# Kernel optimization log

Hardware: AMD Instinct MI355X
Metric: run time of the kernel (lower is better)

Reference implementation:

```python
import jax, jax.numpy as jnp
import numpy as np

N_BINS = 32
R = 1.2
BOUND = 50.0
_m = N_BINS // 2
_x1L = BOUND * (R - 1.0) / (R ** _m - 1.0)
X1L = _x1L / (2.0 * BOUND)  # x1L rescaled to the [0,1] domain
_idx = np.arange(N_BINS + 1, dtype=np.float64) - _m
_xr = np.where(_idx >= 0, (1.0 - R ** _idx) / (1.0 - R), (1.0 - R ** np.abs(_idx)) / (1.0 - R))
_xr = np.where(_idx >= 0, _x1L * _xr, -_x1L * _xr)
_xr = (_xr + BOUND) / (2.0 * BOUND)
MESH = np.concatenate([[0.0], _xr[1:-1], [1.0]]).astype(np.float32)   # (n_bins+1,)
ESIZE = (MESH[1:] - MESH[:-1]).astype(np.float32)                     # (n_bins,)

N, D = 524288, 64

def setup_inputs() -> dict:
    key = jax.random.key(0)
    k1, k2, k3, k4 = jax.random.split(key, 4)
    return {
        "x": jax.random.normal(k1, (N, D), jnp.float32) * 5.0,
        "logdet": jnp.zeros((N, 1), jnp.float32),
        "p": jax.random.normal(k2, (N_BINS - 1, D), jnp.float32) * 0.1,
        "b": jax.random.normal(k3, (1, D), jnp.float32) * 0.1,
        "logs": jax.random.normal(k4, (1, D), jnp.float32) * 0.1,
    }

def reference(x, logdet, p, b, logs):
    mesh = jnp.asarray(MESH)              # (n_bins+1,)
    es = jnp.asarray(ESIZE)               # (n_bins,)
    # ---- actnorm (data_init already done; b_init = logs_init = 0) ----
    ls = jnp.clip(logs, -5.0, 5.0)
    z = (x + b) * jnp.exp(ls)             # (N, D)
    logdet = logdet + jnp.sum(ls)
    # ---- pdf normalization ----
    ep = jnp.exp(p)                                         # (n_bins-1, D)
    w = ((es[:-1] + es[1:]) / 2.0)[:, None]                 # trapezoid weights
    px = ep * ((1.0 - es[0]) / jnp.sum(ep * w, 0, keepdims=True))
    ones = jnp.ones((1, p.shape[1]), p.dtype)
    pdf = jnp.concatenate([ones, px, ones], 0)              # (n_bins+1, D)
    cell = (pdf[:-1] + pdf[1:]) / 2.0 * es[:, None]         # (n_bins, D)
    F_ref = jnp.concatenate([jnp.zeros_like(ones), jnp.cumsum(cell, 0)[:-1]], 0)  # (n_bins, D)
    # ---- forward CDF: analytic bin index + batched gather + quadratic interp ----
    xs = (z + BOUND) / (2.0 * BOUND)                        # map to [0,1]
    sgn = jnp.sign(xs - 0.5)
    mfl = jnp.floor(jnp.log(jnp.abs(xs - 0.5) * (R - 1.0) / X1L + 1.0) / np.log(R))
    k = jnp.where(sgn >= 0, N_BINS // 2 + mfl, N_BINS // 2 - mfl - 1).astype(jnp.int32)
    cover = (k * (k - (N_BINS - 1))) <= 0                   # inside the mesh?
    k = jnp.clip(k, 0, N_BINS - 1)
    v1 = jnp.take_along_axis(pdf, k, 0)                     # pdf at left node
    v2 = jnp.take_along_axis(pdf, k + 1, 0)                 # pdf at right node
    xmodi = xs - mesh[k]
    h = es[k]
    F_pre = jnp.take_along_axis(F_ref, k, 0)
    y = jnp.where(cover, F_pre + xmodi * xmodi * 0.5 * (v2 - v1) / h + xmodi * v1, xs)
    dlog = jnp.where(cover, xmodi * (v2 - v1) / h + v1, 1.0)
    logdet = logdet + jnp.sum(jnp.log(dlog), axis=1, keepdims=True)
    out = y * 2.0 * BOUND - BOUND
    return out, logdet
```

## Files before the change

### kernel.cpp

```cpp
#include <hip/hip_runtime.h>
#include <math.h>

#define NBINS 32
#define DCOLS 64

#define WS_A     0
#define WS_B     2048
#define WS_C     4096
#define WS_S     6144
#define WS_T     6208
#define WS_SUMLS 6272

__global__ __launch_bounds__(64) void precompute_kernel(
    const float* __restrict__ p, const float* __restrict__ b,
    const float* __restrict__ logs, float* __restrict__ ws)
{
  const int d = threadIdx.x;

  double powr[17];
  {
    double rp = 1.0;
    for (int i = 0; i <= 16; i++) { powr[i] = rp; rp *= 1.2; }
  }
  const double x1L = 50.0 * 0.2 / (powr[16] - 1.0);
  float meshf[NBINS + 1];
  for (int i = 0; i <= NBINS; i++) {
    int idx = i - 16;
    int a = idx >= 0 ? idx : -idx;
    double xr = (1.0 - powr[a]) / (1.0 - 1.2);
    xr = (idx >= 0) ? x1L * xr : -x1L * xr;
    meshf[i] = (float)((xr + 50.0) / 100.0);
  }
  meshf[0] = 0.0f;
  meshf[NBINS] = 1.0f;
  float esf[NBINS];
  for (int i = 0; i < NBINS; i++) esf[i] = meshf[i + 1] - meshf[i];

  float ls = logs[d];
  ls = fminf(fmaxf(ls, -5.0f), 5.0f);
  const float s = expf(ls);
  const float bd = b[d];

  float ep[NBINS - 1];
  float denom = 0.0f;
  for (int j = 0; j < NBINS - 1; j++) {
    ep[j] = expf(p[j * DCOLS + d]);
    denom += ep[j] * ((esf[j] + esf[j + 1]) * 0.5f);
  }
  const float fnorm = (1.0f - esf[0]) / denom;
  float pdf[NBINS + 1];
  pdf[0] = 1.0f;
  pdf[NBINS] = 1.0f;
  for (int j = 0; j < NBINS - 1; j++) pdf[j + 1] = ep[j] * fnorm;

  float F = 0.0f;
  for (int k = 0; k < NBINS; k++) {
    const double v1 = (double)pdf[k];
    const double v2 = (double)pdf[k + 1];
    const double h  = (double)esf[k];
    const double m  = (double)meshf[k];
    const double c2 = 0.5 * (v2 - v1) / h;
    const double c1 = v1;
    const double A  = (double)F - c1 * m + c2 * m * m;
    const double B  = c1 - 2.0 * c2 * m;
    ws[WS_A + k * DCOLS + d] = (float)A;
    ws[WS_B + k * DCOLS + d] = (float)B;
    ws[WS_C + k * DCOLS + d] = (float)c2;
    const float cell = 0.5f * (pdf[k] + pdf[k + 1]) * esf[k];
    F += cell;
  }

  ws[WS_S + d] = (float)((double)s * 0.01);
  ws[WS_T + d] = (float)((double)bd * (double)s * 0.01 + 0.5);

  float sum = ls;
  for (int m = 1; m < 64; m <<= 1) sum += __shfl_xor(sum, m, 64);
  if (d == 0) ws[WS_SUMLS] = sum;
}

__device__ __forceinline__ void proc4(
    const float4 xv, const float4 S4, const float4 T4,
    const float* __restrict__ sA, const float* __restrict__ sB,
    const float* __restrict__ sC, int c0, float C1, float INVL2R,
    float4& res, float& prod)
{
  float xs_[4] = { fmaf(xv.x, S4.x, T4.x), fmaf(xv.y, S4.y, T4.y),
                   fmaf(xv.z, S4.z, T4.z), fmaf(xv.w, S4.w, T4.w) };
  float r_[4];
  float pr = 1.0f;
#pragma unroll
  for (int i = 0; i < 4; i++) {
    const float xs = xs_[i];
    const float a  = fabsf(xs - 0.5f);
    const float u  = __log2f(fmaf(a, C1, 1.0f)) * INVL2R;
    const float mfl = floorf(u);
    const float kf  = (xs >= 0.5f) ? (16.0f + mfl) : (15.0f - mfl);
    const int k = (int)kf;
    const bool cover = (k >= 0) && (k <= NBINS - 1);
    const int kc = k < 0 ? 0 : (k > NBINS - 1 ? NBINS - 1 : k);
    const int idx = kc * DCOLS + c0 + i;
    const float Av = sA[idx];
    const float Bv = sB[idx];
    const float Cv = sC[idx];
    const float y  = cover ? fmaf(xs, fmaf(xs, Cv, Bv), Av) : xs;
    const float dl = cover ? fmaf(xs, 2.0f * Cv, Bv) : 1.0f;
    r_[i] = fmaf(y, 100.0f, -50.0f);
    pr *= dl;
  }
  res = make_float4(r_[0], r_[1], r_[2], r_[3]);
  prod = pr;
}

__global__ __launch_bounds__(256) void fwd_kernel(
    const float* __restrict__ x, const float* __restrict__ logdet_in,
    const float* __restrict__ ws, float* __restrict__ out,
    float* __restrict__ logdet_out, int nrows, float C1, float INVL2R)
{
  __shared__ float sA[NBINS * DCOLS];
  __shared__ float sB[NBINS * DCOLS];
  __shared__ float sC[NBINS * DCOLS];
  {
    const float4* wsv = (const float4*)(ws);
    float4* sAv = (float4*)sA;
    float4* sBv = (float4*)sB;
    float4* sCv = (float4*)sC;
    for (int i = threadIdx.x; i < (NBINS * DCOLS) / 4; i += 256) {
      sAv[i] = wsv[(WS_A / 4) + i];
      sBv[i] = wsv[(WS_B / 4) + i];
      sCv[i] = wsv[(WS_C / 4) + i];
    }
  }
  const int lane = threadIdx.x & 63;
  const int wid  = threadIdx.x >> 6;
  const int cg   = lane & 15;
  const int rs   = lane >> 4;
  const int c0   = cg * 4;
  const float4 S4 = *(const float4*)(ws + WS_S + c0);
  const float4 T4 = *(const float4*)(ws + WS_T + c0);
  const float sumls = ws[WS_SUMLS];
  __syncthreads();

  const int gw = blockIdx.x * 4 + wid;
  const int nw = gridDim.x * 4;

  for (int r0 = gw * 8; r0 < nrows; r0 += nw * 8) {
    const int rA = r0 + rs;
    const int rB = r0 + 4 + rs;
    const float4 xA = *(const float4*)(x + (size_t)rA * DCOLS + c0);
    const float4 xB = *(const float4*)(x + (size_t)rB * DCOLS + c0);

    float4 resA, resB;
    float pA, pB;
    proc4(xA, S4, T4, sA, sB, sC, c0, C1, INVL2R, resA, pA);
    proc4(xB, S4, T4, sA, sB, sC, c0, C1, INVL2R, resB, pB);

    *(float4*)(out + (size_t)rA * DCOLS + c0) = resA;
    *(float4*)(out + (size_t)rB * DCOLS + c0) = resB;

#pragma unroll
    for (int m = 1; m < 16; m <<= 1) {
      pA *= __shfl_xor(pA, m, 64);
      pB *= __shfl_xor(pB, m, 64);
    }
    if (cg == 0) {
      logdet_out[rA] = logdet_in[rA] + sumls + logf(pA);
      logdet_out[rB] = logdet_in[rB] + sumls + logf(pB);
    }
  }
}

extern "C" void kernel_launch(void* const* d_in, const int* in_sizes, int n_in,
                              void* d_out, int out_size, void* d_ws, size_t ws_size,
                              hipStream_t stream) {
  const float* x      = (const float*)d_in[0];
  const float* logdet = (const float*)d_in[1];
  const float* p      = (const float*)d_in[2];
  const float* b      = (const float*)d_in[3];
  const float* logs   = (const float*)d_in[4];
  float* out = (float*)d_out;
  float* ws  = (float*)d_ws;

  const int N = in_sizes[0] / DCOLS;
  float* logdet_out = out + (size_t)N * DCOLS;

  precompute_kernel<<<1, 64, 0, stream>>>(p, b, logs, ws);

  double Rm = 1.0;
  for (int i = 0; i < 16; i++) Rm *= 1.2;
  const double x1L = 50.0 * (1.2 - 1.0) / (Rm - 1.0);
  const double X1L = x1L / 100.0;
  const float C1      = (float)((1.2 - 1.0) / X1L);
  const float INVL2R  = (float)(1.0 / log2(1.2));

  const int grid = 2048;
  fwd_kernel<<<grid, 256, 0, stream>>>(x, logdet, ws, out, logdet_out, N,
                                       C1, INVL2R);
}
```

Baseline: 250.9 us.

## Swizzle LDS coefficient tables and process four row groups per iteration

Coefficient tables are stored with a column swizzle (d -> (d&3)*16 + d/4). Within a float4 component, the 16 column-group lanes then read consecutive LDS words instead of a stride of 4, which is meant to cut bank conflicts on the per-element gathers. The main loop also handles 16 rows per wave per iteration instead of 8, giving four independent loads in flight per lane. The wider unroll raises register use and halves the number of loop iterations per wave.

Result: no change. 248.9 us (-0.8%).

```diff
diff --git a/kernel.cpp b/kernel.cpp
--- a/kernel.cpp
+++ b/kernel.cpp
@@ -11,11 +11,14 @@
 #define WS_T     6208
 #define WS_SUMLS 6272
 
+__device__ __forceinline__ int swz(int d) { return ((d & 3) << 4) | (d >> 2); }
+
 __global__ __launch_bounds__(64) void precompute_kernel(
     const float* __restrict__ p, const float* __restrict__ b,
     const float* __restrict__ logs, float* __restrict__ ws)
 {
   const int d = threadIdx.x;
+  const int ds = swz(d);
 
   double powr[17];
   {
@@ -63,9 +66,9 @@
     const double c1 = v1;
     const double A  = (double)F - c1 * m + c2 * m * m;
     const double B  = c1 - 2.0 * c2 * m;
-    ws[WS_A + k * DCOLS + d] = (float)A;
-    ws[WS_B + k * DCOLS + d] = (float)B;
-    ws[WS_C + k * DCOLS + d] = (float)c2;
+    ws[WS_A + k * DCOLS + ds] = (float)A;
+    ws[WS_B + k * DCOLS + ds] = (float)B;
+    ws[WS_C + k * DCOLS + ds] = (float)c2;
     const float cell = 0.5f * (pdf[k] + pdf[k + 1]) * esf[k];
     F += cell;
   }
@@ -81,7 +84,7 @@
 __device__ __forceinline__ void proc4(
     const float4 xv, const float4 S4, const float4 T4,
     const float* __restrict__ sA, const float* __restrict__ sB,
-    const float* __restrict__ sC, int c0, float C1, float INVL2R,
+    const float* __restrict__ sC, int cg, float C1, float INVL2R,
     float4& res, float& prod)
 {
   float xs_[4] = { fmaf(xv.x, S4.x, T4.x), fmaf(xv.y, S4.y, T4.y),
@@ -98,7 +101,7 @@
     const int k = (int)kf;
     const bool cover = (k >= 0) && (k <= NBINS - 1);
     const int kc = k < 0 ? 0 : (k > NBINS - 1 ? NBINS - 1 : k);
-    const int idx = kc * DCOLS + c0 + i;
+    const int idx = kc * DCOLS + 16 * i + cg;
     const float Av = sA[idx];
     const float Bv = sB[idx];
     const float Cv = sC[idx];
@@ -143,28 +146,40 @@
   const int gw = blockIdx.x * 4 + wid;
   const int nw = gridDim.x * 4;
 
-  for (int r0 = gw * 8; r0 < nrows; r0 += nw * 8) {
+  for (int r0 = gw * 16; r0 < nrows; r0 += nw * 16) {
     const int rA = r0 + rs;
     const int rB = r0 + 4 + rs;
+    const int rC = r0 + 8 + rs;
+    const int rD = r0 + 12 + rs;
     const float4 xA = *(const float4*)(x + (size_t)rA * DCOLS + c0);
     const float4 xB = *(const float4*)(x + (size_t)rB * DCOLS + c0);
-
-    float4 resA, resB;
-    float pA, pB;
-    proc4(xA, S4, T4, sA, sB, sC, c0, C1, INVL2R, resA, pA);
-    proc4(xB, S4, T4, sA, sB, sC, c0, C1, INVL2R, resB, pB);
+    const float4 xC = *(const float4*)(x + (size_t)rC * DCOLS + c0);
+    const float4 xD = *(const float4*)(x + (size_t)rD * DCOLS + c0);
+
+    float4 resA, resB, resC, resD;
+    float pA, pB, pC, pD;
+    proc4(xA, S4, T4, sA, sB, sC, cg, C1, INVL2R, resA, pA);
+    proc4(xB, S4, T4, sA, sB, sC, cg, C1, INVL2R, resB, pB);
+    proc4(xC, S4, T4, sA, sB, sC, cg, C1, INVL2R, resC, pC);
+    proc4(xD, S4, T4, sA, sB, sC, cg, C1, INVL2R, resD, pD);
 
     *(float4*)(out + (size_t)rA * DCOLS + c0) = resA;
     *(float4*)(out + (size_t)rB * DCOLS + c0) = resB;
+    *(float4*)(out + (size_t)rC * DCOLS + c0) = resC;
+    *(float4*)(out + (size_t)rD * DCOLS + c0) = resD;
 
 #pragma unroll
     for (int m = 1; m < 16; m <<= 1) {
       pA *= __shfl_xor(pA, m, 64);
       pB *= __shfl_xor(pB, m, 64);
+      pC *= __shfl_xor(pC, m, 64);
+      pD *= __shfl_xor(pD, m, 64);
     }
     if (cg == 0) {
       logdet_out[rA] = logdet_in[rA] + sumls + logf(pA);
       logdet_out[rB] = logdet_in[rB] + sumls + logf(pB);
+      logdet_out[rC] = logdet_in[rC] + sumls + logf(pC);
+      logdet_out[rD] = logdet_in[rD] + sumls + logf(pD);
     }
   }
 }
```
